# Performance work log

Measured on AMD Instinct MI355X. Metric: run time of the kernel, lower is better.

## Reference

```python
import jax, jax.numpy as jnp
import numpy as np

D_MODEL = 2048
NUM_Q_HEADS = 32
NUM_KV_HEADS = 8
HEAD_SIZE = 64
GROUP_SIZE = NUM_Q_HEADS // NUM_KV_HEADS
B, T = 2, 2048


def setup_inputs() -> dict:
    key = jax.random.key(0)
    k0, k1, k2, k3 = jax.random.split(key, 4)
    std = 1.0 / np.sqrt(D_MODEL)
    x = jax.random.normal(k0, (B, T, D_MODEL), dtype=jnp.float32)
    Wq = jax.random.normal(k1, (D_MODEL, NUM_Q_HEADS * HEAD_SIZE), dtype=jnp.float32) * std
    Wk = jax.random.normal(k2, (D_MODEL, NUM_KV_HEADS * HEAD_SIZE), dtype=jnp.float32) * std
    Wv = jax.random.normal(k3, (D_MODEL, NUM_KV_HEADS * HEAD_SIZE), dtype=jnp.float32) * std
    return {"x": x, "Wq": Wq, "Wk": Wk, "Wv": Wv}


def reference(x, Wq, Wk, Wv):
    Bs, Ts, _ = x.shape
    scale = jnp.sqrt(jnp.asarray(HEAD_SIZE, dtype=x.dtype))
    # projections -> [B, H, T, D]
    q = (x @ Wq).reshape(Bs, Ts, NUM_Q_HEADS, HEAD_SIZE).transpose(0, 2, 1, 3)
    k = (x @ Wk).reshape(Bs, Ts, NUM_KV_HEADS, HEAD_SIZE).transpose(0, 2, 1, 3)
    v = (x @ Wv).reshape(Bs, Ts, NUM_KV_HEADS, HEAD_SIZE).transpose(0, 2, 1, 3)
    # repeat kv heads to match q heads (GQA)
    k = jnp.repeat(k, GROUP_SIZE, axis=1)  # [B, Hq, T, D]
    v = jnp.repeat(v, GROUP_SIZE, axis=1)
    scores = jnp.einsum('bhqd,bhkd->bhqk', q, k) / scale  # [B, Hq, T, T]
    causal = jnp.tril(jnp.ones((Ts, Ts), dtype=bool))
    scores = jnp.where(causal, scores, -jnp.inf)
    attn = jax.nn.softmax(scores, axis=-1)
    out = jnp.einsum('bhqk,bhkd->bhqd', attn, v)  # [B, Hq, T, D]
    return out.transpose(0, 2, 1, 3).reshape(Bs, Ts, NUM_Q_HEADS * HEAD_SIZE)
```

## Files before the change

kernel.cpp:

```cpp
#include <hip/hip_runtime.h>

typedef float floatx4 __attribute__((ext_vector_type(4)));
typedef short shortx8 __attribute__((ext_vector_type(8)));

#define T_SEQ 2048
#define NQH   32
#define NKVH  8
#define HD    64
#define DM    2048
#define NTOT  3072

#if __has_builtin(__builtin_amdgcn_exp2f)
#define EXP2F(x) __builtin_amdgcn_exp2f(x)
#else
#define EXP2F(x) exp2f(x)
#endif

__device__ __forceinline__ unsigned short f2bf(float f) {
    unsigned int u = __builtin_bit_cast(unsigned int, f);
    u += 0x7FFFu + ((u >> 16) & 1u);
    return (unsigned short)(u >> 16);
}
__device__ __forceinline__ unsigned int pk2bf(float a, float b) {
    return (unsigned int)f2bf(a) | ((unsigned int)f2bf(b) << 16);
}

__device__ __forceinline__ unsigned int cvtpk_bf16(float lo, float hi) {
    unsigned int r;
    asm("v_cvt_pk_bf16_f32 %0, %1, %2" : "=v"(r) : "v"(lo), "v"(hi));
    return r;
}

__device__ __forceinline__ void dma16(const unsigned short* g, unsigned short* l) {
    __builtin_amdgcn_global_load_lds(
        (const __attribute__((address_space(1))) unsigned int*)g,
        (__attribute__((address_space(3))) unsigned int*)l,
        16, 0, 0);
}

__global__ __launch_bounds__(256) void cvt_fused(
    const float* __restrict__ x, const float* __restrict__ Wq,
    const float* __restrict__ Wk, const float* __restrict__ Wv,
    unsigned short* __restrict__ xb, unsigned short* __restrict__ wt)
{
    __shared__ __align__(16) unsigned short Ts[64][72];
    const int id = blockIdx.x;
    const int t = threadIdx.x;
    if (id < 4096) {
        size_t i = ((size_t)id * 256 + t) * 8;
        float4 a = *(const float4*)(x + i);
        float4 b = *(const float4*)(x + i + 4);
        uint4 o;
        o.x = pk2bf(a.x, a.y); o.y = pk2bf(a.z, a.w);
        o.z = pk2bf(b.x, b.y); o.w = pk2bf(b.z, b.w);
        *(uint4*)(xb + i) = o;
        return;
    }
    const int id2 = id - 4096;
    const int k0 = (id2 & 31) * 64, n0g = (id2 >> 5) * 64;
    const float* W; int ldW, col0;
    if (n0g < 2048)      { W = Wq; ldW = 2048; col0 = n0g; }
    else if (n0g < 2560) { W = Wk; ldW = 512;  col0 = n0g - 2048; }
    else                 { W = Wv; ldW = 512;  col0 = n0g - 2560; }
    {
        int r = t >> 2, c = (t & 3) * 16;
        const float* src = W + (size_t)(k0 + r) * ldW + col0 + c;
        float4 v0 = *(const float4*)(src);
        float4 v1 = *(const float4*)(src + 4);
        float4 v2 = *(const float4*)(src + 8);
        float4 v3 = *(const float4*)(src + 12);
        uint4 o0 = {pk2bf(v0.x, v0.y), pk2bf(v0.z, v0.w), pk2bf(v1.x, v1.y), pk2bf(v1.z, v1.w)};
        uint4 o1 = {pk2bf(v2.x, v2.y), pk2bf(v2.z, v2.w), pk2bf(v3.x, v3.y), pk2bf(v3.z, v3.w)};
        *(uint4*)&Ts[r][c]     = o0;
        *(uint4*)&Ts[r][c + 8] = o1;
    }
    __syncthreads();
    {
        int n = t >> 2, kc = (t & 3) * 16;
        unsigned int dw[8];
        #pragma unroll
        for (int i = 0; i < 8; i++)
            dw[i] = (unsigned int)Ts[kc + 2 * i][n] | ((unsigned int)Ts[kc + 2 * i + 1][n] << 16);
        uint4 o0 = {dw[0], dw[1], dw[2], dw[3]}, o1 = {dw[4], dw[5], dw[6], dw[7]};
        unsigned short* d = wt + (size_t)(n0g + n) * DM + k0 + kc;
        *(uint4*)d = o0; *(uint4*)(d + 8) = o1;
    }
}

__global__ __launch_bounds__(256, 4) void qkv_gemm(
    const unsigned short* __restrict__ xb,
    const unsigned short* __restrict__ wt,
    unsigned short* __restrict__ Qws, unsigned short* __restrict__ Kws,
    unsigned short* __restrict__ Vws)
{
    __shared__ __align__(16) unsigned short At[128 * 64];
    __shared__ __align__(16) unsigned short Bt[128 * 64];

    const int tid = threadIdx.x;
    const int wave = tid >> 6, lane = tid & 63;
    const int l16 = lane & 15, qd = lane >> 4;

    const int id  = blockIdx.y * 24 + blockIdx.x;
    const int xcd = id & 7, j = id >> 3;
    const int m0 = (xcd * 4 + (j & 3)) * 128;
    const int n0 = (j >> 2) * 128;

    const int mh = (wave >> 1) * 64, nh = (wave & 1) * 64;

    const int lrow = lane >> 3;
    const int cgw  = (lane & 7) ^ lrow;
    const int cg0  = (qd ^ (l16 & 7)) * 8;
    const int cg1  = ((4 | qd) ^ (l16 & 7)) * 8;

    floatx4 acc[4][4];
    #pragma unroll
    for (int mi = 0; mi < 4; mi++)
        #pragma unroll
        for (int ni = 0; ni < 4; ni++)
            acc[mi][ni] = (floatx4){0.f, 0.f, 0.f, 0.f};

    size_t gA[4], gB[4];
    int lofs[4];
    #pragma unroll
    for (int jj = 0; jj < 4; jj++) {
        const int rb = wave * 32 + jj * 8;
        gA[jj] = (size_t)(m0 + rb + lrow) * DM + cgw * 8;
        gB[jj] = (size_t)(n0 + rb + lrow) * DM + cgw * 8;
        lofs[jj] = rb * 64;
    }

    #pragma unroll
    for (int jj = 0; jj < 4; jj++) {
        dma16(xb + gA[jj], &At[lofs[jj]]);
        dma16(wt + gB[jj], &Bt[lofs[jj]]);
    }

    for (int k0 = 0; k0 < DM; k0 += 64) {
        __syncthreads();
        #pragma unroll
        for (int ks = 0; ks < 2; ks++) {
            const int cg = ks ? cg1 : cg0;
            shortx8 af[4], bfr[4];
            #pragma unroll
            for (int i = 0; i < 4; i++) {
                af[i]  = *(const shortx8*)&At[(mh + i * 16 + l16) * 64 + cg];
                bfr[i] = *(const shortx8*)&Bt[(nh + i * 16 + l16) * 64 + cg];
            }
            #pragma unroll
            for (int mi = 0; mi < 4; mi++)
                #pragma unroll
                for (int ni = 0; ni < 4; ni++)
                    acc[mi][ni] = __builtin_amdgcn_mfma_f32_16x16x32_bf16(
                        af[mi], bfr[ni], acc[mi][ni], 0, 0, 0);
        }
        __syncthreads();
        if (k0 + 64 < DM) {
            #pragma unroll
            for (int jj = 0; jj < 4; jj++) {
                dma16(xb + gA[jj] + k0 + 64, &At[lofs[jj]]);
                dma16(wt + gB[jj] + k0 + 64, &Bt[lofs[jj]]);
            }
        }
    }

    int ncol, H; unsigned short* dst; float sc; bool vtrans;
    if (n0 < 2048)      { ncol = n0;        dst = Qws; H = NQH;  sc = 0.125f * 1.44269504f; vtrans = false; }
    else if (n0 < 2560) { ncol = n0 - 2048; dst = Kws; H = NKVH; sc = 1.0f; vtrans = false; }
    else                { ncol = n0 - 2560; dst = Vws; H = NKVH; sc = 1.0f; vtrans = true;  }

    #pragma unroll
    for (int mi = 0; mi < 4; mi++)
        #pragma unroll
        for (int ni = 0; ni < 4; ni++)
            #pragma unroll
            for (int r = 0; r < 4; r++) {
                int m  = m0 + mh + mi * 16 + qd * 4 + r;
                int nc = ncol + nh + ni * 16 + l16;
                int b  = m >> 11, t = m & (T_SEQ - 1);
                int hh = nc >> 6, d = nc & 63;
                float v = acc[mi][ni][r] * sc;
                size_t idx = vtrans
                    ? ((((size_t)b * H + hh) * HD + d) << 11) + t
                    : ((((size_t)b * H + hh) * T_SEQ + t) << 6) + d;
                dst[idx] = f2bf(v);
            }
}

__global__ __launch_bounds__(512, 4) void attn_fwd(
    const unsigned short* __restrict__ Qws,
    const unsigned short* __restrict__ Kws,
    const unsigned short* __restrict__ Vtws,
    float* __restrict__ out)
{
    __shared__ __align__(16) unsigned short Ks[2][64 * 64];
    __shared__ __align__(16) unsigned short Vt[2][64 * 64];
    __shared__ __align__(16) unsigned short Ps[8][32][40];

    const int tid = threadIdx.x;
    const int wave = tid >> 6, lane = tid & 63;
    const int whead = wave & 3, wrow = wave >> 2;
    const int l16 = lane & 15, qd = lane >> 4;
    const int b = blockIdx.z;
    const int qt = b ? blockIdx.x : (31 - blockIdx.x);
    const int kh = blockIdx.y;
    const int h = kh * 4 + whead;
    const int q0 = qt * 64;
    const int mh = wrow * 32;

    const size_t qbase  = (((size_t)b * NQH + h) * T_SEQ + q0) * HD;
    const size_t kbase  = ((size_t)b * NKVH + kh) * (size_t)T_SEQ * HD;
    const size_t vtbase = ((size_t)b * NKVH + kh) * (size_t)HD * T_SEQ;

    shortx8 qfr[2][2];
    #pragma unroll
    for (int mqt = 0; mqt < 2; mqt++)
        #pragma unroll
        for (int ks = 0; ks < 2; ks++)
            qfr[mqt][ks] = *(const shortx8*)(Qws + qbase +
                (size_t)(mh + mqt * 16 + l16) * HD + ks * 32 + qd * 8);

    const shortx8 ones = {0x3F80, 0x3F80, 0x3F80, 0x3F80,
                          0x3F80, 0x3F80, 0x3F80, 0x3F80};

    floatx4 oaccT[2][4];
    #pragma unroll
    for (int mqt = 0; mqt < 2; mqt++)
        #pragma unroll
        for (int dt = 0; dt < 4; dt++)
            oaccT[mqt][dt] = (floatx4){0.f, 0.f, 0.f, 0.f};
    floatx4 psum[2];
    psum[0] = (floatx4){0.f, 0.f, 0.f, 0.f};
    psum[1] = (floatx4){0.f, 0.f, 0.f, 0.f};

    const int lrow = lane >> 3;
    const int cgw  = (lane & 7) ^ lrow;
    const int xr   = l16 & 7;
    const int rb   = wave * 8;

    dma16(Kws  + kbase  + (size_t)(rb + lrow) * HD + cgw * 8, &Ks[0][rb * 64]);
    dma16(Vtws + vtbase + (size_t)(rb + lrow) * T_SEQ + cgw * 8, &Vt[0][rb * 64]);

    for (int c = 0; c <= qt; c++) {
        const int cur = c & 1;
        __syncthreads();
        if (c < qt) {
            const int j0n = (c + 1) * 64;
            dma16(Kws  + kbase  + (size_t)(j0n + rb + lrow) * HD + cgw * 8,
                  &Ks[cur ^ 1][rb * 64]);
            dma16(Vtws + vtbase + (size_t)(rb + lrow) * T_SEQ + j0n + cgw * 8,
                  &Vt[cur ^ 1][rb * 64]);
        }

        const bool diag = (c == qt);

        #pragma unroll
        for (int kp = 0; kp < 2; kp++) {
            if (!(diag && wrow == 0 && kp == 1)) {
                shortx8 kf[2][2];
                #pragma unroll
                for (int ktl = 0; ktl < 2; ktl++) {
                    const int krow = ((kp * 2 + ktl) * 16 + l16) * 64;
                    kf[ktl][0] = *(const shortx8*)&Ks[cur][krow + ((qd ^ xr) * 8)];
                    kf[ktl][1] = *(const shortx8*)&Ks[cur][krow + (((4 | qd) ^ xr) * 8)];
                }

                const bool msk = diag && (wrow == kp);

                #pragma unroll
                for (int ktl = 0; ktl < 2; ktl++) {
                    #pragma unroll
                    for (int mqt = 0; mqt < 2; mqt++) {
                        floatx4 s = (floatx4){0.f, 0.f, 0.f, 0.f};
                        s = __builtin_amdgcn_mfma_f32_16x16x32_bf16(kf[ktl][0], qfr[mqt][0], s, 0, 0, 0);
                        s = __builtin_amdgcn_mfma_f32_16x16x32_bf16(kf[ktl][1], qfr[mqt][1], s, 0, 0, 0);
                        float pe[4];
                        #pragma unroll
                        for (int r = 0; r < 4; r++) pe[r] = EXP2F(s[r]);
                        if (msk) {
                            const int qrel  = mh + mqt * 16 + l16;
                            const int jbase = kp * 32 + ktl * 16 + qd * 4;
                            #pragma unroll
                            for (int r = 0; r < 4; r++)
                                if (jbase + r > qrel) pe[r] = 0.f;
                        }
                        uint2 dw;
                        dw.x = cvtpk_bf16(pe[0], pe[1]);
                        dw.y = cvtpk_bf16(pe[2], pe[3]);
                        *(uint2*)&Ps[wave][mqt * 16 + l16][ktl * 16 + qd * 4] = dw;
                    }
                }

                shortx8 pfr[2];
                #pragma unroll
                for (int mqt = 0; mqt < 2; mqt++)
                    pfr[mqt] = *(const shortx8*)&Ps[wave][mqt * 16 + l16][qd * 8];

                #pragma unroll
                for (int mqt = 0; mqt < 2; mqt++)
                    psum[mqt] = __builtin_amdgcn_mfma_f32_16x16x32_bf16(
                        ones, pfr[mqt], psum[mqt], 0, 0, 0);

                __builtin_amdgcn_s_setprio(1);
                #pragma unroll
                for (int dt = 0; dt < 4; dt++) {
                    const shortx8 vf = *(const shortx8*)
                        &Vt[cur][(dt * 16 + l16) * 64 + (((kp * 4 + qd) ^ xr) * 8)];
                    #pragma unroll
                    for (int mqt = 0; mqt < 2; mqt++)
                        oaccT[mqt][dt] = __builtin_amdgcn_mfma_f32_16x16x32_bf16(
                            vf, pfr[mqt], oaccT[mqt][dt], 0, 0, 0);
                }
                __builtin_amdgcn_s_setprio(0);
            }
        }
    }

    float inv[2];
    inv[0] = 1.f / psum[0][0];
    inv[1] = 1.f / psum[1][0];

    #pragma unroll
    for (int mqt = 0; mqt < 2; mqt++) {
        const int t = q0 + mh + mqt * 16 + l16;
        float* orow = out + ((size_t)b * T_SEQ + t) * (NQH * HD) + h * HD + qd * 4;
        #pragma unroll
        for (int dt = 0; dt < 4; dt++) {
            float4 o;
            o.x = oaccT[mqt][dt][0] * inv[mqt];
            o.y = oaccT[mqt][dt][1] * inv[mqt];
            o.z = oaccT[mqt][dt][2] * inv[mqt];
            o.w = oaccT[mqt][dt][3] * inv[mqt];
            *(float4*)(orow + dt * 16) = o;
        }
    }
}

extern "C" void kernel_launch(void* const* d_in, const int* in_sizes, int n_in,
                              void* d_out, int out_size, void* d_ws, size_t ws_size,
                              hipStream_t stream) {
    const float* x  = (const float*)d_in[0];
    const float* Wq = (const float*)d_in[1];
    const float* Wk = (const float*)d_in[2];
    const float* Wv = (const float*)d_in[3];
    float* out = (float*)d_out;

    unsigned short* xb  = (unsigned short*)d_out;
    unsigned short* wt  = (unsigned short*)d_ws;
    unsigned short* Qws = wt  + (size_t)NTOT * DM;
    unsigned short* Kws = Qws + (size_t)2 * NQH * T_SEQ * HD;
    unsigned short* Vws = Kws + (size_t)2 * NKVH * T_SEQ * HD;

    cvt_fused<<<4096 + 1536, 256, 0, stream>>>(x, Wq, Wk, Wv, xb, wt);
    qkv_gemm <<<dim3(24, 32), 256, 0, stream>>>(xb, wt, Qws, Kws, Vws);
    attn_fwd <<<dim3(32, NKVH, 2), 512, 0, stream>>>(Qws, Kws, Vws, out);
}
```

Before: 213.4 us.

## Retile QKV GEMM to 256x192 tiles with double-buffered phased DMA pipeline

The QKV projection GEMM moves from 128x128 tiles with 256 threads and a single LDS buffer to 256x192 tiles with 512 threads. The grid becomes 256 workgroups, one per CU, with an XCD-aware mapping. LDS is double-buffered, and loads for the next k-tile are split across four MFMA phases with fine-grained vmcnt waits, barriers and s_setprio, so global-to-LDS traffic overlaps compute. The larger tile improves data reuse but raises LDS use (about 112KB) and register pressure, and the epilogue now branches per column to Q/K/V.

```diff
diff --git a/kernel.cpp b/kernel.cpp
--- a/kernel.cpp
+++ b/kernel.cpp
@@ -87,103 +87,135 @@
     }
 }
 
-__global__ __launch_bounds__(256, 4) void qkv_gemm(
+__global__ __launch_bounds__(512, 2) void qkv_gemm(
     const unsigned short* __restrict__ xb,
     const unsigned short* __restrict__ wt,
     unsigned short* __restrict__ Qws, unsigned short* __restrict__ Kws,
     unsigned short* __restrict__ Vws)
 {
-    __shared__ __align__(16) unsigned short At[128 * 64];
-    __shared__ __align__(16) unsigned short Bt[128 * 64];
+    __shared__ __align__(16) unsigned short At[2][256 * 64];
+    __shared__ __align__(16) unsigned short Bt[2][192 * 64];
 
     const int tid = threadIdx.x;
     const int wave = tid >> 6, lane = tid & 63;
     const int l16 = lane & 15, qd = lane >> 4;
-
-    const int id  = blockIdx.y * 24 + blockIdx.x;
+    const int wm = wave >> 2, wn = wave & 3;
+
+    const int id  = blockIdx.x;
     const int xcd = id & 7, j = id >> 3;
-    const int m0 = (xcd * 4 + (j & 3)) * 128;
-    const int n0 = (j >> 2) * 128;
-
-    const int mh = (wave >> 1) * 64, nh = (wave & 1) * 64;
+    const int wg  = xcd * 32 + j;
+    const int mt  = wg >> 4, nt = wg & 15;
+    const int m0 = mt * 256, n0g = nt * 192;
 
     const int lrow = lane >> 3;
     const int cgw  = (lane & 7) ^ lrow;
     const int cg0  = (qd ^ (l16 & 7)) * 8;
     const int cg1  = ((4 | qd) ^ (l16 & 7)) * 8;
 
-    floatx4 acc[4][4];
-    #pragma unroll
-    for (int mi = 0; mi < 4; mi++)
-        #pragma unroll
-        for (int ni = 0; ni < 4; ni++)
+    floatx4 acc[8][3];
+    #pragma unroll
+    for (int mi = 0; mi < 8; mi++)
+        #pragma unroll
+        for (int ni = 0; ni < 3; ni++)
             acc[mi][ni] = (floatx4){0.f, 0.f, 0.f, 0.f};
 
-    size_t gA[4], gB[4];
-    int lofs[4];
-    #pragma unroll
-    for (int jj = 0; jj < 4; jj++) {
-        const int rb = wave * 32 + jj * 8;
-        gA[jj] = (size_t)(m0 + rb + lrow) * DM + cgw * 8;
-        gB[jj] = (size_t)(n0 + rb + lrow) * DM + cgw * 8;
-        lofs[jj] = rb * 64;
-    }
-
-    #pragma unroll
-    for (int jj = 0; jj < 4; jj++) {
-        dma16(xb + gA[jj], &At[lofs[jj]]);
-        dma16(wt + gB[jj], &Bt[lofs[jj]]);
-    }
-
-    for (int k0 = 0; k0 < DM; k0 += 64) {
-        __syncthreads();
-        #pragma unroll
-        for (int ks = 0; ks < 2; ks++) {
-            const int cg = ks ? cg1 : cg0;
-            shortx8 af[4], bfr[4];
+    const unsigned short* gA = xb + (size_t)(m0 + wave * 8 + lrow) * DM + cgw * 8;
+    const unsigned short* gB = wt + (size_t)(n0g + wave * 8 + lrow) * DM + cgw * 8;
+
+#define DMA_A(s, kt, b) dma16(gA + (size_t)(s) * 64 * DM + (kt) * 64, \
+                              &At[b][(s) * 4096 + wave * 512])
+#define DMA_B(s, kt, b) dma16(gB + (size_t)(s) * 64 * DM + (kt) * 64, \
+                              &Bt[b][(s) * 4096 + wave * 512])
+
+    DMA_B(0, 0, 0); DMA_B(1, 0, 0); DMA_B(2, 0, 0);
+    DMA_A(0, 0, 0); DMA_A(2, 0, 0); DMA_A(1, 0, 0); DMA_A(3, 0, 0);
+
+    shortx8 bfr[3][2], af[2][2];
+
+#define PH_LOAD_A(q) { \
+    _Pragma("unroll") for (int mf = 0; mf < 2; mf++) { \
+        const int ar = (wm * 128 + (q) * 32 + mf * 16 + l16) * 64; \
+        af[mf][0] = *(const shortx8*)&At[cur][ar + cg0]; \
+        af[mf][1] = *(const shortx8*)&At[cur][ar + cg1]; } }
+
+#define PH_MFMA(q) { __builtin_amdgcn_s_setprio(1); \
+    _Pragma("unroll") for (int mf = 0; mf < 2; mf++) \
+    _Pragma("unroll") for (int nf = 0; nf < 3; nf++) { \
+        acc[(q) * 2 + mf][nf] = __builtin_amdgcn_mfma_f32_16x16x32_bf16( \
+            af[mf][0], bfr[nf][0], acc[(q) * 2 + mf][nf], 0, 0, 0); \
+        acc[(q) * 2 + mf][nf] = __builtin_amdgcn_mfma_f32_16x16x32_bf16( \
+            af[mf][1], bfr[nf][1], acc[(q) * 2 + mf][nf], 0, 0, 0); } \
+    __builtin_amdgcn_s_setprio(0); }
+
+    int cur = 0;
+    for (int kt = 0; kt < 32; ++kt) {
+        const bool pf = (kt < 31);
+        const int nb = cur ^ 1;
+
+        asm volatile("s_waitcnt vmcnt(2)" ::: "memory");
+        __builtin_amdgcn_s_barrier();
+        asm volatile("" ::: "memory");
+
+        #pragma unroll
+        for (int nf = 0; nf < 3; nf++) {
+            const int bn = (wn * 48 + nf * 16 + l16) * 64;
+            bfr[nf][0] = *(const shortx8*)&Bt[cur][bn + cg0];
+            bfr[nf][1] = *(const shortx8*)&Bt[cur][bn + cg1];
+        }
+        PH_LOAD_A(0)
+        if (pf) { DMA_B(0, kt + 1, nb); DMA_B(1, kt + 1, nb); }
+        PH_MFMA(0)
+        __builtin_amdgcn_s_barrier();
+
+        PH_LOAD_A(1)
+        if (pf) { DMA_B(2, kt + 1, nb); DMA_A(0, kt + 1, nb); }
+        PH_MFMA(1)
+
+        if (pf) asm volatile("s_waitcnt vmcnt(4)" ::: "memory");
+        else    asm volatile("s_waitcnt vmcnt(0)" ::: "memory");
+        __builtin_amdgcn_s_barrier();
+        asm volatile("" ::: "memory");
+
+        PH_LOAD_A(2)
+        if (pf) { DMA_A(2, kt + 1, nb); DMA_A(1, kt + 1, nb); }
+        PH_MFMA(2)
+        __builtin_amdgcn_s_barrier();
+
+        PH_LOAD_A(3)
+        if (pf) { DMA_A(3, kt + 1, nb); }
+        PH_MFMA(3)
+
+        cur = nb;
+    }
+
+    const float qsc = 0.125f * 1.44269504f;
+    #pragma unroll
+    for (int q = 0; q < 4; q++)
+        #pragma unroll
+        for (int mf = 0; mf < 2; mf++)
             #pragma unroll
-            for (int i = 0; i < 4; i++) {
-                af[i]  = *(const shortx8*)&At[(mh + i * 16 + l16) * 64 + cg];
-                bfr[i] = *(const shortx8*)&Bt[(nh + i * 16 + l16) * 64 + cg];
-            }
-            #pragma unroll
-            for (int mi = 0; mi < 4; mi++)
-                #pragma unroll
-                for (int ni = 0; ni < 4; ni++)
-                    acc[mi][ni] = __builtin_amdgcn_mfma_f32_16x16x32_bf16(
-                        af[mi], bfr[ni], acc[mi][ni], 0, 0, 0);
-        }
-        __syncthreads();
-        if (k0 + 64 < DM) {
-            #pragma unroll
-            for (int jj = 0; jj < 4; jj++) {
-                dma16(xb + gA[jj] + k0 + 64, &At[lofs[jj]]);
-                dma16(wt + gB[jj] + k0 + 64, &Bt[lofs[jj]]);
-            }
-        }
-    }
-
-    int ncol, H; unsigned short* dst; float sc; bool vtrans;
-    if (n0 < 2048)      { ncol = n0;        dst = Qws; H = NQH;  sc = 0.125f * 1.44269504f; vtrans = false; }
-    else if (n0 < 2560) { ncol = n0 - 2048; dst = Kws; H = NKVH; sc = 1.0f; vtrans = false; }
-    else                { ncol = n0 - 2560; dst = Vws; H = NKVH; sc = 1.0f; vtrans = true;  }
-
-    #pragma unroll
-    for (int mi = 0; mi < 4; mi++)
-        #pragma unroll
-        for (int ni = 0; ni < 4; ni++)
-            #pragma unroll
-            for (int r = 0; r < 4; r++) {
-                int m  = m0 + mh + mi * 16 + qd * 4 + r;
-                int nc = ncol + nh + ni * 16 + l16;
-                int b  = m >> 11, t = m & (T_SEQ - 1);
-                int hh = nc >> 6, d = nc & 63;
-                float v = acc[mi][ni][r] * sc;
-                size_t idx = vtrans
-                    ? ((((size_t)b * H + hh) * HD + d) << 11) + t
-                    : ((((size_t)b * H + hh) * T_SEQ + t) << 6) + d;
-                dst[idx] = f2bf(v);
-            }
+            for (int nf = 0; nf < 3; nf++)
+                #pragma unroll
+                for (int r = 0; r < 4; r++) {
+                    int m   = m0 + wm * 128 + q * 32 + mf * 16 + qd * 4 + r;
+                    int ncg = n0g + wn * 48 + nf * 16 + l16;
+                    int b   = m >> 11, t = m & (T_SEQ - 1);
+                    float v = acc[q * 2 + mf][nf][r];
+                    if (ncg < 2048) {
+                        int hh = ncg >> 6, d = ncg & 63;
+                        Qws[((((size_t)b * NQH + hh) * T_SEQ + t) << 6) + d] = f2bf(v * qsc);
+                    } else if (ncg < 2560) {
+                        int nc = ncg - 2048, hh = nc >> 6, d = nc & 63;
+                        Kws[((((size_t)b * NKVH + hh) * T_SEQ + t) << 6) + d] = f2bf(v);
+                    } else {
+                        int nc = ncg - 2560, hh = nc >> 6, d = nc & 63;
+                        Vws[((((size_t)b * NKVH + hh) * HD + d) << 11) + t] = f2bf(v);
+                    }
+                }
+#undef DMA_A
+#undef DMA_B
+#undef PH_LOAD_A
+#undef PH_MFMA
 }
 
 __global__ __launch_bounds__(512, 4) void attn_fwd(
@@ -351,6 +383,6 @@
     unsigned short* Vws = Kws + (size_t)2 * NKVH * T_SEQ * HD;
 
     cvt_fused<<<4096 + 1536, 256, 0, stream>>>(x, Wq, Wk, Wv, xb, wt);
-    qkv_gemm <<<dim3(24, 32), 256, 0, stream>>>(xb, wt, Qws, Kws, Vws);
+    qkv_gemm <<<256, 512, 0, stream>>>(xb, wt, Qws, Kws, Vws);
     attn_fwd <<<dim3(32, NKVH, 2), 512, 0, stream>>>(Qws, Kws, Vws, out);
 }
```

New measurement: 221.0 us. 1.04x slower.
